# Kernel tuning notes

Hardware: AMD Instinct MI355X
Metric: run time of the kernel (lower is better)

The kernel has to match this reference:

```python
import jax, jax.numpy as jnp
import numpy as np

N_NODES = 50000
N_EDGES = 300000
HID = 256


def setup_inputs() -> dict:
    key = jax.random.key(0)
    ks = jax.random.split(key, 8)
    s = lambda fan_in: 1.0 / np.sqrt(fan_in)
    return {
        "node_embeddings": jax.random.normal(ks[0], (N_NODES, HID), dtype=jnp.float32),
        "edge_index": jax.random.randint(ks[1], (2, N_EDGES), 0, N_NODES, dtype=jnp.int64),
        "edge_attr": jax.random.normal(ks[2], (N_EDGES, 3), dtype=jnp.float32),
        "W1": jax.random.normal(ks[3], (2 * HID + 3, HID), dtype=jnp.float32) * s(2 * HID + 3),
        "b1": jnp.zeros((HID,), dtype=jnp.float32),
        "W2": jax.random.normal(ks[4], (HID, HID // 2), dtype=jnp.float32) * s(HID),
        "b2": jnp.zeros((HID // 2,), dtype=jnp.float32),
        "W3": jax.random.normal(ks[5], (HID // 2, HID // 4), dtype=jnp.float32) * s(HID // 2),
        "b3": jnp.zeros((HID // 4,), dtype=jnp.float32),
        "W4": jax.random.normal(ks[6], (HID // 4, 3), dtype=jnp.float32) * s(HID // 4),
        "b4": jnp.zeros((3,), dtype=jnp.float32),
    }


def reference(node_embeddings, edge_index, edge_attr, W1, b1, W2, b2, W3, b3, W4, b4):
    # Gather source/target node embeddings: [E, H] each
    src = node_embeddings[edge_index[0]]
    dst = node_embeddings[edge_index[1]]
    feats = jnp.concatenate([src, dst, edge_attr], axis=-1)  # [E, 2H+3]
    # edge_encoder: Linear -> ReLU -> (Dropout=identity in eval) -> Linear
    h = jax.nn.relu(feats @ W1 + b1)
    h = h @ W2 + b2  # [E, H//2]
    # classifier: Linear -> ReLU -> Linear
    h = jax.nn.relu(h @ W3 + b3)
    logits = h @ W4 + b4  # [E, 3]
    return logits
```

## Files before the change

kernel.cpp:

```cpp
#include <hip/hip_runtime.h>
#include <hip/hip_bf16.h>
#include <stdint.h>
#include <stddef.h>


#define NN 50000
#define NE 300000
#define KG(kq,g2) ((kq)*2+(g2))

using bf16x8 = __attribute__((ext_vector_type(8))) short;
using f32x16 = __attribute__((ext_vector_type(16))) float;
using f32x4  = __attribute__((ext_vector_type(4))) float;
using f32x2  = __attribute__((ext_vector_type(2))) float;
using u32x4  = __attribute__((ext_vector_type(4))) unsigned int;
using u32x2  = __attribute__((ext_vector_type(2))) unsigned int;

#define OFF_PQ   0ULL
#define SZ_PQ    (50000ULL*512ULL*2ULL)
#define OFF_W1   (OFF_PQ + SZ_PQ)
#define SZ_W1    (512ULL*256ULL*2ULL)
#define OFF_W1C  (OFF_W1 + SZ_W1)
#define SZ_W1C   (3ULL*256ULL*4ULL)
#define OFF_W2   (OFF_W1C + SZ_W1C)
#define SZ_W2    (128ULL*256ULL*2ULL)
#define OFF_W3   (OFF_W2 + SZ_W2)
#define SZ_W3    (64ULL*128ULL*2ULL)
#define OFF_W4   (OFF_W3 + SZ_W3)
#define SZ_W4    (16ULL*64ULL*2ULL)
#define OFF_FLAG (OFF_W4 + SZ_W4)
#define WS_NEED  (OFF_FLAG + 16ULL)

__device__ __forceinline__ unsigned short f2bf(float x){
  unsigned u = __float_as_uint(x);
  unsigned r = 0x7FFFu + ((u >> 16) & 1u);
  return (unsigned short)((u + r) >> 16);
}
__device__ __forceinline__ unsigned cvtpk(float lo, float hi){
  unsigned r;
  asm("v_cvt_pk_bf16_f32 %0, %1, %2" : "=v"(r) : "v"(lo), "v"(hi));
  return r;
}
__device__ __forceinline__ f32x2 unpk(unsigned w){
  f32x2 r;
  r[0] = __uint_as_float(w << 16);
  r[1] = __uint_as_float(w & 0xFFFF0000u);
  return r;
}
__device__ __forceinline__ f32x16 mfma32(bf16x8 a, bf16x8 b, f32x16 c){
  return __builtin_amdgcn_mfma_f32_32x32x16_bf16(a, b, c, 0, 0, 0);
}
__device__ __forceinline__ f32x4 mfma16(bf16x8 a, bf16x8 b, f32x4 c){
  return __builtin_amdgcn_mfma_f32_16x16x32_bf16(a, b, c, 0, 0, 0);
}
__device__ __forceinline__ f32x16 zero16(){
  f32x16 v;
#pragma unroll
  for (int i = 0; i < 16; ++i) v[i] = 0.f;
  return v;
}

__global__ void prep_pack(const float* __restrict__ W1, const float* __restrict__ W2,
                          const float* __restrict__ W3, const float* __restrict__ W4,
                          const int* __restrict__ ei32, char* __restrict__ ws)
{
  int i = blockIdx.x * 256 + threadIdx.x;
  unsigned short* w1i = (unsigned short*)(ws + OFF_W1);
  unsigned short* w2i = (unsigned short*)(ws + OFF_W2);
  unsigned short* w3i = (unsigned short*)(ws + OFF_W3);
  unsigned short* w4i = (unsigned short*)(ws + OFF_W4);

  if (i < 131072){
    int j = i & 7, out = (i >> 3) & 511, kg = i >> 12;
    int k = (kg >> 1)*16 + (kg & 1)*8 + j;
    float v = (out < 256) ? W1[(size_t)k*256 + out]
                          : W1[(size_t)(256 + k)*256 + (out - 256)];
    w1i[i] = f2bf(v);
  } else if (i < 131072 + 32768){
    int i2 = i - 131072;
    int j = i2 & 7, out = (i2 >> 3) & 127, sg = i2 >> 10;
    int k = (sg >> 2)*32 + (sg & 3)*8 + j;
    w2i[i2] = f2bf(W2[(size_t)k*128 + out]);
  } else if (i < 131072 + 32768 + 8192){
    int i3 = i - 131072 - 32768;
    int j = i3 & 7, out = (i3 >> 3) & 63, sg = i3 >> 9;
    int k = (sg >> 2)*32 + (sg & 3)*8 + j;
    w3i[i3] = f2bf(W3[(size_t)k*64 + out]);
  } else if (i < 131072 + 32768 + 8192 + 1024){
    int i4 = i - 131072 - 32768 - 8192;
    int j = i4 & 7, out = (i4 >> 3) & 15, sg = i4 >> 7;
    int k = (sg >> 2)*32 + (sg & 3)*8 + j;
    w4i[i4] = (out < 3) ? f2bf(W4[(size_t)k*3 + out]) : (unsigned short)0;
  }
  if (i < 768){
    float* w1c = (float*)(ws + OFF_W1C);
    w1c[i] = W1[(size_t)(512 + i/256)*256 + (i & 255)];
  }
  if (i == 0){
    int f = 1;
    for (int t = 1; t < 64; t += 2) if (ei32[t] != 0) { f = 0; break; }
    *(int*)(ws + OFF_FLAG) = f;
  }
}

__global__ __launch_bounds__(512, 2) void gemm1(const float* __restrict__ emb,
                                                const float* __restrict__ b1,
                                                char* __restrict__ ws)
{
  __shared__ __align__(16) unsigned short U[16896];

  const int tid = threadIdx.x;
  const int wv = tid >> 6, l = tid & 63, ln = l & 31, g2 = l >> 5;
  const int nb = blockIdx.x * 64;
  const int ob = wv * 64;
  const unsigned short* w1L = (const unsigned short*)(ws + OFF_W1);
  unsigned short* PQ = (unsigned short*)(ws + OFF_PQ);

  bf16x8 aw[2][16];
#pragma unroll
  for (int kq = 0; kq < 16; ++kq){
#pragma unroll
    for (int t2 = 0; t2 < 2; ++t2)
      aw[t2][kq] = *(const bf16x8*)(w1L + ((size_t)KG(kq,g2)*512 + ob + t2*32 + ln)*8);
  }

#pragma unroll
  for (int it = 0; it < 8; ++it){
    int u = it*512 + tid;
    int kg = u >> 7, node = (u >> 1) & 63, half = u & 1;
    int n = nb + node; if (n >= NN) n = NN - 1;
    int k = (kg >> 1)*16 + (kg & 1)*8 + half*4;
    f32x4 e = *(const f32x4*)(emb + (size_t)n*256 + k);
    u32x2 w; w[0] = cvtpk(e[0], e[1]); w[1] = cvtpk(e[2], e[3]);
    *(u32x2*)(U + (size_t)kg*512 + node*8 + half*4) = w;
  }
  __syncthreads();

  f32x16 acc[2][2];
  acc[0][0] = zero16(); acc[0][1] = zero16();
  acc[1][0] = zero16(); acc[1][1] = zero16();
#pragma unroll
  for (int kq = 0; kq < 16; ++kq){
    bf16x8 b0  = *(const bf16x8*)(U + ((size_t)KG(kq,g2)*64 +      ln)*8);
    bf16x8 b1v = *(const bf16x8*)(U + ((size_t)KG(kq,g2)*64 + 32 + ln)*8);
    acc[0][0] = mfma32(aw[0][kq], b0,  acc[0][0]);
    acc[1][0] = mfma32(aw[1][kq], b0,  acc[1][0]);
    acc[0][1] = mfma32(aw[0][kq], b1v, acc[0][1]);
    acc[1][1] = mfma32(aw[1][kq], b1v, acc[1][1]);
  }
  __syncthreads();

  const int r_ = tid >> 4;
  const int j_ = tid & 15;
#define G1PASS(BG)                                                             \
  {                                                                            \
           \
    _Pragma("unroll")                                                          \
    for (int t2 = 0; t2 < 2; ++t2){                                            \
      _Pragma("unroll")                                                        \
      for (int rr = 0; rr < 4; ++rr){                                          \
        int o = ob + t2*32 + rr*8 + g2*4;                                      \
        f32x4 bv = {0.f,0.f,0.f,0.f};                                          \
        if (ob + t2*32 < 256) bv = *(const f32x4*)(b1 + o);                    \
        unsigned d0 = cvtpk(acc[t2][BG][rr*4+0]+bv[0], acc[t2][BG][rr*4+1]+bv[1]); \
        unsigned d1 = cvtpk(acc[t2][BG][rr*4+2]+bv[2], acc[t2][BG][rr*4+3]+bv[3]); \
        u32x2 st = {d0, d1};                                                   \
        *(u32x2*)(U + (size_t)ln*516 + o) = st;                                \
      }                                                                        \
    }                                                                          \
    __syncthreads();                                                           \
                            \
    {                                                                          \
      int n = nb + (BG)*32 + r_;                                               \
      if (n < NN){                                                             \
        _Pragma("unroll")                                                      \
        for (int ii = 0; ii < 4; ++ii){                                        \
          uint4 v = *(const uint4*)(U + (size_t)r_*516 + ii*128 + j_*8);       \
          *(uint4*)(PQ + (size_t)n*512 + ii*128 + j_*8) = v;                   \
        }                                                                      \
      }                                                                        \
    }                                                                          \
  }
  G1PASS(0);
  __syncthreads();
  G1PASS(1);
#undef G1PASS
}


#define PAIRX(LO, HI, D) ((D)==0 ? (f32x2){(LO)[0],(LO)[1]} : \
                          (D)==1 ? (f32x2){(LO)[2],(LO)[3]} : \
                          (D)==2 ? (f32x2){(HI)[0],(HI)[1]} : \
                                   (f32x2){(HI)[2],(HI)[3]})

#define H1BUILD(PC, QC, A0, A1, A2, BOUT)                                      \
  {                                                                            \
    u32x4 pu = __builtin_bit_cast(u32x4, PC);                                  \
    u32x4 qu = __builtin_bit_cast(u32x4, QC);                                  \
    f32x2 z2 = {0.f, 0.f};                                                     \
    unsigned bu0, bu1, bu2, bu3;                                               \
    _Pragma("unroll")                                                          \
    for (int d = 0; d < 4; ++d){                                               \
      f32x2 h = unpk(pu[d]) + unpk(qu[d]);                                     \
      h += PAIRX(w0lo, w0hi, d) * (A0);                                        \
      h += PAIRX(w1lo, w1hi, d) * (A1);                                        \
      h += PAIRX(w2lo, w2hi, d) * (A2);                                        \
      h = __builtin_elementwise_max(h, z2);                                    \
      unsigned c = cvtpk(h[0], h[1]);                                          \
      if (d==0) bu0 = c; else if (d==1) bu1 = c; else if (d==2) bu2 = c;       \
      else bu3 = c;                                                            \
    }                                                                          \
    u32x4 buv = {bu0, bu1, bu2, bu3};                                          \
    BOUT = __builtin_bit_cast(bf16x8, buv);                                    \
  }

#define L2S(S, P0, Q0, P1, Q1)                                                 \
  {                                                                            \
    const int kb = (S)*32 + g4*8;                                              \
    f32x4 w0lo = *(const f32x4*)(w1c_lds +   0 + kb);                          \
    f32x4 w0hi = *(const f32x4*)(w1c_lds +   4 + kb);                          \
    f32x4 w1lo = *(const f32x4*)(w1c_lds + 256 + kb);                          \
    f32x4 w1hi = *(const f32x4*)(w1c_lds + 260 + kb);                          \
    f32x4 w2lo = *(const f32x4*)(w1c_lds + 512 + kb);                          \
    f32x4 w2hi = *(const f32x4*)(w1c_lds + 516 + kb);                          \
    bf16x8 b0, b1;                                                             \
    H1BUILD(P0, Q0, at0e0, at1e0, at2e0, b0);                                  \
    H1BUILD(P1, Q1, at0e1, at1e1, at2e1, b1);                                  \
    if ((S) + 2 <= 7){                                                         \
      P0 = *(const bf16x8*)(Prow0 + ((S)+2)*32);                               \
      Q0 = *(const bf16x8*)(Qrow0 + ((S)+2)*32);                               \
      P1 = *(const bf16x8*)(Prow1 + ((S)+2)*32);                               \
      Q1 = *(const bf16x8*)(Qrow1 + ((S)+2)*32);                               \
    }                                                                          \
    const char* abase = smem + (size_t)((S)*4 + g4)*2048 + c16*16;             \
    _Pragma("unroll")                                                          \
    for (int t = 0; t < 8; ++t){                                               \
      bf16x8 af = *(const bf16x8*)(abase + t*256);                             \
      acc2[t][0] = mfma16(af, b0, acc2[t][0]);                                 \
      acc2[t][1] = mfma16(af, b1, acc2[t][1]);                                 \
    }                                                                          \
  }

__global__ __launch_bounds__(512, 4) void fused(const int* __restrict__ eidx,
                                                const float* __restrict__ attr,
                                                const float* __restrict__ b2,
                                                const float* __restrict__ b3,
                                                const float* __restrict__ b4,
                                                const char* __restrict__ ws,
                                                float* __restrict__ out)
{
  __shared__ __align__(16) char smem[65536 + 3072];
  const int tid = threadIdx.x;
  const int wv = tid >> 6, l = tid & 63, c16 = l & 15, g4 = l >> 4;

  const unsigned short* PQ  = (const unsigned short*)(ws + OFF_PQ);
  const unsigned short* w3g = (const unsigned short*)(ws + OFF_W3);
  const unsigned short* w4g = (const unsigned short*)(ws + OFF_W4);
  const float* W1c = (const float*)(ws + OFF_W1C);
  const int flag64 = *(const int*)(ws + OFF_FLAG);
  const float* w1c_lds = (const float*)(smem + 65536);

  const int ebase = blockIdx.x * 256 + wv * 32;
  const int e0 = ebase + c16,      e1 = ebase + 16 + c16;
  const bool ev0 = (e0 < NE),      ev1 = (e1 < NE);
  const int ec0 = ev0 ? e0 : 0,    ec1 = ev1 ? e1 : 0;
  const int si0 = flag64 ? eidx[2*(size_t)ec0]        : eidx[ec0];
  const int di0 = flag64 ? eidx[2*((size_t)NE + ec0)] : eidx[NE + ec0];
  const int si1 = flag64 ? eidx[2*(size_t)ec1]        : eidx[ec1];
  const int di1 = flag64 ? eidx[2*((size_t)NE + ec1)] : eidx[NE + ec1];

  const float at0e0 = ev0 ? attr[(size_t)ec0*3 + 0] : 0.f;
  const float at1e0 = ev0 ? attr[(size_t)ec0*3 + 1] : 0.f;
  const float at2e0 = ev0 ? attr[(size_t)ec0*3 + 2] : 0.f;
  const float at0e1 = ev1 ? attr[(size_t)ec1*3 + 0] : 0.f;
  const float at1e1 = ev1 ? attr[(size_t)ec1*3 + 1] : 0.f;
  const float at2e1 = ev1 ? attr[(size_t)ec1*3 + 2] : 0.f;

  const unsigned short* Prow0 = PQ + (size_t)si0*512 + g4*8;
  const unsigned short* Qrow0 = PQ + (size_t)di0*512 + 256 + g4*8;
  const unsigned short* Prow1 = PQ + (size_t)si1*512 + g4*8;
  const unsigned short* Qrow1 = PQ + (size_t)di1*512 + 256 + g4*8;

  bf16x8 pA0 = *(const bf16x8*)(Prow0 +  0), qA0 = *(const bf16x8*)(Qrow0 +  0);
  bf16x8 pA1 = *(const bf16x8*)(Prow1 +  0), qA1 = *(const bf16x8*)(Qrow1 +  0);
  bf16x8 pB0 = *(const bf16x8*)(Prow0 + 32), qB0 = *(const bf16x8*)(Qrow0 + 32);
  bf16x8 pB1 = *(const bf16x8*)(Prow1 + 32), qB1 = *(const bf16x8*)(Qrow1 + 32);

  {
    const uint4* src = (const uint4*)(ws + OFF_W2);
    uint4* dst = (uint4*)smem;
#pragma unroll
    for (int it = 0; it < 8; ++it) dst[it*512 + tid] = src[it*512 + tid];
    if (tid < 192) ((f32x4*)(smem + 65536))[tid] = ((const f32x4*)W1c)[tid];
  }
  __syncthreads();

  f32x4 acc2[8][2];
#pragma unroll
  for (int t = 0; t < 8; ++t){ acc2[t][0] = (f32x4){0,0,0,0}; acc2[t][1] = (f32x4){0,0,0,0}; }

  L2S(0, pA0, qA0, pA1, qA1);
  L2S(1, pB0, qB0, pB1, qB1);
  L2S(2, pA0, qA0, pA1, qA1);
  L2S(3, pB0, qB0, pB1, qB1);
  L2S(4, pA0, qA0, pA1, qA1);
  L2S(5, pB0, qB0, pB1, qB1);
  L2S(6, pA0, qA0, pA1, qA1);
  L2S(7, pB0, qB0, pB1, qB1);

  __syncthreads();

  unsigned short* hslot = (unsigned short*)(smem + wv*8192);
#pragma unroll
  for (int t = 0; t < 8; ++t){
    f32x4 bv = *(const f32x4*)(b2 + t*16 + g4*4);
    const int sg_o = t*2 + (g4 >> 1);
    const int j0 = (g4 & 1)*4;
#pragma unroll
    for (int g = 0; g < 2; ++g){
      unsigned d0 = cvtpk(acc2[t][g][0]+bv[0], acc2[t][g][1]+bv[1]);
      unsigned d1 = cvtpk(acc2[t][g][2]+bv[2], acc2[t][g][3]+bv[3]);
      u32x2 st = {d0, d1};
      *(u32x2*)(hslot + ((sg_o*32 + g*16 + c16)*8 + j0)) = st;
    }
  }

  f32x4 acc3[4][2];
#pragma unroll
  for (int t = 0; t < 4; ++t){ acc3[t][0] = (f32x4){0,0,0,0}; acc3[t][1] = (f32x4){0,0,0,0}; }
#pragma unroll
  for (int ks = 0; ks < 4; ++ks){
    const int sg = ks*4 + g4;
    bf16x8 bb0 = *(const bf16x8*)(hslot + (sg*32 +      c16)*8);
    bf16x8 bb1 = *(const bf16x8*)(hslot + (sg*32 + 16 + c16)*8);
#pragma unroll
    for (int t = 0; t < 4; ++t){
      bf16x8 af = *(const bf16x8*)(w3g + ((size_t)sg*64 + t*16 + c16)*8);
      acc3[t][0] = mfma16(af, bb0, acc3[t][0]);
      acc3[t][1] = mfma16(af, bb1, acc3[t][1]);
    }
  }

#pragma unroll
  for (int t = 0; t < 4; ++t){
    f32x4 bv = *(const f32x4*)(b3 + t*16 + g4*4);
    const int sg_o = t*2 + (g4 >> 1);
    const int j0 = (g4 & 1)*4;
#pragma unroll
    for (int g = 0; g < 2; ++g){
      unsigned d0 = cvtpk(fmaxf(acc3[t][g][0]+bv[0],0.f), fmaxf(acc3[t][g][1]+bv[1],0.f));
      unsigned d1 = cvtpk(fmaxf(acc3[t][g][2]+bv[2],0.f), fmaxf(acc3[t][g][3]+bv[3],0.f));
      u32x2 st = {d0, d1};
      *(u32x2*)(hslot + ((sg_o*32 + g*16 + c16)*8 + j0)) = st;
    }
  }

  f32x4 acc40 = {0,0,0,0}, acc41 = {0,0,0,0};
#pragma unroll
  for (int ks = 0; ks < 2; ++ks){
    const int sg = ks*4 + g4;
    bf16x8 af = *(const bf16x8*)(w4g + ((size_t)sg*16 + c16)*8);
    bf16x8 bb0 = *(const bf16x8*)(hslot + (sg*32 +      c16)*8);
    bf16x8 bb1 = *(const bf16x8*)(hslot + (sg*32 + 16 + c16)*8);
    acc40 = mfma16(af, bb0, acc40);
    acc41 = mfma16(af, bb1, acc41);
  }
  if (g4 == 0){
    float c0 = b4[0], c1 = b4[1], c2 = b4[2];
    if (ev0){
      out[(size_t)e0*3 + 0] = acc40[0] + c0;
      out[(size_t)e0*3 + 1] = acc40[1] + c1;
      out[(size_t)e0*3 + 2] = acc40[2] + c2;
    }
    if (ev1){
      out[(size_t)e1*3 + 0] = acc41[0] + c0;
      out[(size_t)e1*3 + 1] = acc41[1] + c1;
      out[(size_t)e1*3 + 2] = acc41[2] + c2;
    }
  }
}

extern "C" void kernel_launch(void* const* d_in, const int* in_sizes, int n_in,
                              void* d_out, int out_size, void* d_ws, size_t ws_size,
                              hipStream_t stream)
{
  const float* emb  = (const float*)d_in[0];
  const int*   eidx = (const int*)  d_in[1];
  const float* attr = (const float*)d_in[2];
  const float* W1   = (const float*)d_in[3];
  const float* b1   = (const float*)d_in[4];
  const float* W2   = (const float*)d_in[5];
  const float* b2   = (const float*)d_in[6];
  const float* W3   = (const float*)d_in[7];
  const float* b3   = (const float*)d_in[8];
  const float* W4   = (const float*)d_in[9];
  const float* b4   = (const float*)d_in[10];
  char* ws = (char*)d_ws;
  float* out = (float*)d_out;

  if (ws_size < WS_NEED) return;

  prep_pack<<<676, 256, 0, stream>>>(W1, W2, W3, W4, eidx, ws);
  gemm1<<<(NN + 63)/64, 512, 0, stream>>>(emb, b1, ws);
  fused<<<(NE + 255)/256, 512, 0, stream>>>(eidx, attr, b2, b3, b4, ws, out);
}
```

Measured before the change: 116.7 us.

## Move small weight packing into gemm1, process two node tiles per block, add setprio

Packing of the W2, W3, W4 and W1-tail weights moves out of prep_pack into extra blocks of gemm1, so prep_pack only converts W1. Each gemm1 block now handles two 64-node tiles in a loop, so the W1 fragments held in registers are loaded once and reused across both tiles. The grid shrinks to about one wave of blocks. The fused kernel wraps its MFMA loops in s_setprio to favour matrix issue. The risks are less parallelism in gemm1 and extra synchronisation, and the setprio effect depends on how waves interleave.

```diff
diff --git a/kernel.cpp b/kernel.cpp
--- a/kernel.cpp
+++ b/kernel.cpp
@@ -7,6 +7,7 @@
 #define NN 50000
 #define NE 300000
 #define KG(kq,g2) ((kq)*2+(g2))
+#define NBG1 391
 
 using bf16x8 = __attribute__((ext_vector_type(8))) short;
 using f32x16 = __attribute__((ext_vector_type(16))) float;
@@ -59,41 +60,17 @@
   return v;
 }
 
-__global__ void prep_pack(const float* __restrict__ W1, const float* __restrict__ W2,
-                          const float* __restrict__ W3, const float* __restrict__ W4,
+__global__ void prep_pack(const float* __restrict__ W1,
                           const int* __restrict__ ei32, char* __restrict__ ws)
 {
   int i = blockIdx.x * 256 + threadIdx.x;
   unsigned short* w1i = (unsigned short*)(ws + OFF_W1);
-  unsigned short* w2i = (unsigned short*)(ws + OFF_W2);
-  unsigned short* w3i = (unsigned short*)(ws + OFF_W3);
-  unsigned short* w4i = (unsigned short*)(ws + OFF_W4);
-
   if (i < 131072){
     int j = i & 7, out = (i >> 3) & 511, kg = i >> 12;
     int k = (kg >> 1)*16 + (kg & 1)*8 + j;
     float v = (out < 256) ? W1[(size_t)k*256 + out]
                           : W1[(size_t)(256 + k)*256 + (out - 256)];
     w1i[i] = f2bf(v);
-  } else if (i < 131072 + 32768){
-    int i2 = i - 131072;
-    int j = i2 & 7, out = (i2 >> 3) & 127, sg = i2 >> 10;
-    int k = (sg >> 2)*32 + (sg & 3)*8 + j;
-    w2i[i2] = f2bf(W2[(size_t)k*128 + out]);
-  } else if (i < 131072 + 32768 + 8192){
-    int i3 = i - 131072 - 32768;
-    int j = i3 & 7, out = (i3 >> 3) & 63, sg = i3 >> 9;
-    int k = (sg >> 2)*32 + (sg & 3)*8 + j;
-    w3i[i3] = f2bf(W3[(size_t)k*64 + out]);
-  } else if (i < 131072 + 32768 + 8192 + 1024){
-    int i4 = i - 131072 - 32768 - 8192;
-    int j = i4 & 7, out = (i4 >> 3) & 15, sg = i4 >> 7;
-    int k = (sg >> 2)*32 + (sg & 3)*8 + j;
-    w4i[i4] = (out < 3) ? f2bf(W4[(size_t)k*3 + out]) : (unsigned short)0;
-  }
-  if (i < 768){
-    float* w1c = (float*)(ws + OFF_W1C);
-    w1c[i] = W1[(size_t)(512 + i/256)*256 + (i & 255)];
   }
   if (i == 0){
     int f = 1;
@@ -104,13 +81,45 @@
 
 __global__ __launch_bounds__(512, 2) void gemm1(const float* __restrict__ emb,
                                                 const float* __restrict__ b1,
+                                                const float* __restrict__ W1,
+                                                const float* __restrict__ W2,
+                                                const float* __restrict__ W3,
+                                                const float* __restrict__ W4,
                                                 char* __restrict__ ws)
 {
   __shared__ __align__(16) unsigned short U[16896];
 
   const int tid = threadIdx.x;
+  const int bid = blockIdx.x;
+
+  if (bid >= NBG1){
+    int p = (bid - NBG1)*512 + tid;
+    unsigned short* w2i = (unsigned short*)(ws + OFF_W2);
+    unsigned short* w3i = (unsigned short*)(ws + OFF_W3);
+    unsigned short* w4i = (unsigned short*)(ws + OFF_W4);
+    float* w1c = (float*)(ws + OFF_W1C);
+    if (p < 32768){
+      int j = p & 7, out = (p >> 3) & 127, sg = p >> 10;
+      int k = (sg >> 2)*32 + (sg & 3)*8 + j;
+      w2i[p] = f2bf(W2[(size_t)k*128 + out]);
+    } else if (p < 40960){
+      int i3 = p - 32768;
+      int j = i3 & 7, out = (i3 >> 3) & 63, sg = i3 >> 9;
+      int k = (sg >> 2)*32 + (sg & 3)*8 + j;
+      w3i[i3] = f2bf(W3[(size_t)k*64 + out]);
+    } else if (p < 41984){
+      int i4 = p - 40960;
+      int j = i4 & 7, out = (i4 >> 3) & 15, sg = i4 >> 7;
+      int k = (sg >> 2)*32 + (sg & 3)*8 + j;
+      w4i[i4] = (out < 3) ? f2bf(W4[(size_t)k*3 + out]) : (unsigned short)0;
+    } else if (p < 42752){
+      int i5 = p - 41984;
+      w1c[i5] = W1[(size_t)(512 + i5/256)*256 + (i5 & 255)];
+    }
+    return;
+  }
+
   const int wv = tid >> 6, l = tid & 63, ln = l & 31, g2 = l >> 5;
-  const int nb = blockIdx.x * 64;
   const int ob = wv * 64;
   const unsigned short* w1L = (const unsigned short*)(ws + OFF_W1);
   unsigned short* PQ = (unsigned short*)(ws + OFF_PQ);
@@ -123,67 +132,71 @@
       aw[t2][kq] = *(const bf16x8*)(w1L + ((size_t)KG(kq,g2)*512 + ob + t2*32 + ln)*8);
   }
 
-#pragma unroll
-  for (int it = 0; it < 8; ++it){
-    int u = it*512 + tid;
-    int kg = u >> 7, node = (u >> 1) & 63, half = u & 1;
-    int n = nb + node; if (n >= NN) n = NN - 1;
-    int k = (kg >> 1)*16 + (kg & 1)*8 + half*4;
-    f32x4 e = *(const f32x4*)(emb + (size_t)n*256 + k);
-    u32x2 w; w[0] = cvtpk(e[0], e[1]); w[1] = cvtpk(e[2], e[3]);
-    *(u32x2*)(U + (size_t)kg*512 + node*8 + half*4) = w;
-  }
-  __syncthreads();
-
-  f32x16 acc[2][2];
-  acc[0][0] = zero16(); acc[0][1] = zero16();
-  acc[1][0] = zero16(); acc[1][1] = zero16();
-#pragma unroll
-  for (int kq = 0; kq < 16; ++kq){
-    bf16x8 b0  = *(const bf16x8*)(U + ((size_t)KG(kq,g2)*64 +      ln)*8);
-    bf16x8 b1v = *(const bf16x8*)(U + ((size_t)KG(kq,g2)*64 + 32 + ln)*8);
-    acc[0][0] = mfma32(aw[0][kq], b0,  acc[0][0]);
-    acc[1][0] = mfma32(aw[1][kq], b0,  acc[1][0]);
-    acc[0][1] = mfma32(aw[0][kq], b1v, acc[0][1]);
-    acc[1][1] = mfma32(aw[1][kq], b1v, acc[1][1]);
-  }
-  __syncthreads();
-
-  const int r_ = tid >> 4;
-  const int j_ = tid & 15;
+#pragma unroll 1
+  for (int rep = 0; rep < 2; ++rep){
+    const int nb = (bid*2 + rep) * 64;
+    __syncthreads();
+
+#pragma unroll
+    for (int it = 0; it < 8; ++it){
+      int u = it*512 + tid;
+      int kg = u >> 7, node = (u >> 1) & 63, half = u & 1;
+      int n = nb + node; if (n >= NN) n = NN - 1;
+      int k = (kg >> 1)*16 + (kg & 1)*8 + half*4;
+      f32x4 e = *(const f32x4*)(emb + (size_t)n*256 + k);
+      u32x2 w; w[0] = cvtpk(e[0], e[1]); w[1] = cvtpk(e[2], e[3]);
+      *(u32x2*)(U + (size_t)kg*512 + node*8 + half*4) = w;
+    }
+    __syncthreads();
+
+    f32x16 acc[2][2];
+    acc[0][0] = zero16(); acc[0][1] = zero16();
+    acc[1][0] = zero16(); acc[1][1] = zero16();
+#pragma unroll
+    for (int kq = 0; kq < 16; ++kq){
+      bf16x8 b0  = *(const bf16x8*)(U + ((size_t)KG(kq,g2)*64 +      ln)*8);
+      bf16x8 b1v = *(const bf16x8*)(U + ((size_t)KG(kq,g2)*64 + 32 + ln)*8);
+      acc[0][0] = mfma32(aw[0][kq], b0,  acc[0][0]);
+      acc[1][0] = mfma32(aw[1][kq], b0,  acc[1][0]);
+      acc[0][1] = mfma32(aw[0][kq], b1v, acc[0][1]);
+      acc[1][1] = mfma32(aw[1][kq], b1v, acc[1][1]);
+    }
+    __syncthreads();
+
+    const int r_ = tid >> 4;
+    const int j_ = tid & 15;
 #define G1PASS(BG)                                                             \
-  {                                                                            \
-           \
-    _Pragma("unroll")                                                          \
-    for (int t2 = 0; t2 < 2; ++t2){                                            \
+    {                                                                          \
       _Pragma("unroll")                                                        \
-      for (int rr = 0; rr < 4; ++rr){                                          \
-        int o = ob + t2*32 + rr*8 + g2*4;                                      \
-        f32x4 bv = {0.f,0.f,0.f,0.f};                                          \
-        if (ob + t2*32 < 256) bv = *(const f32x4*)(b1 + o);                    \
-        unsigned d0 = cvtpk(acc[t2][BG][rr*4+0]+bv[0], acc[t2][BG][rr*4+1]+bv[1]); \
-        unsigned d1 = cvtpk(acc[t2][BG][rr*4+2]+bv[2], acc[t2][BG][rr*4+3]+bv[3]); \
-        u32x2 st = {d0, d1};                                                   \
-        *(u32x2*)(U + (size_t)ln*516 + o) = st;                                \
-      }                                                                        \
-    }                                                                          \
-    __syncthreads();                                                           \
-                            \
-    {                                                                          \
-      int n = nb + (BG)*32 + r_;                                               \
-      if (n < NN){                                                             \
+      for (int t2 = 0; t2 < 2; ++t2){                                          \
         _Pragma("unroll")                                                      \
-        for (int ii = 0; ii < 4; ++ii){                                        \
-          uint4 v = *(const uint4*)(U + (size_t)r_*516 + ii*128 + j_*8);       \
-          *(uint4*)(PQ + (size_t)n*512 + ii*128 + j_*8) = v;                   \
+        for (int rr = 0; rr < 4; ++rr){                                        \
+          int o = ob + t2*32 + rr*8 + g2*4;                                    \
+          f32x4 bv = {0.f,0.f,0.f,0.f};                                        \
+          if (ob + t2*32 < 256) bv = *(const f32x4*)(b1 + o);                  \
+          unsigned d0 = cvtpk(acc[t2][BG][rr*4+0]+bv[0], acc[t2][BG][rr*4+1]+bv[1]); \
+          unsigned d1 = cvtpk(acc[t2][BG][rr*4+2]+bv[2], acc[t2][BG][rr*4+3]+bv[3]); \
+          u32x2 st = {d0, d1};                                                 \
+          *(u32x2*)(U + (size_t)ln*516 + o) = st;                              \
         }                                                                      \
       }                                                                        \
-    }                                                                          \
-  }
-  G1PASS(0);
-  __syncthreads();
-  G1PASS(1);
+      __syncthreads();                                                         \
+      {                                                                        \
+        int n = nb + (BG)*32 + r_;                                             \
+        if (n < NN){                                                           \
+          _Pragma("unroll")                                                    \
+          for (int ii = 0; ii < 4; ++ii){                                      \
+            uint4 v = *(const uint4*)(U + (size_t)r_*516 + ii*128 + j_*8);     \
+            *(uint4*)(PQ + (size_t)n*512 + ii*128 + j_*8) = v;                 \
+          }                                                                    \
+        }                                                                      \
+      }                                                                        \
+    }
+    G1PASS(0);
+    __syncthreads();
+    G1PASS(1);
 #undef G1PASS
+  }
 }
 
 
@@ -232,12 +245,14 @@
       Q1 = *(const bf16x8*)(Qrow1 + ((S)+2)*32);                               \
     }                                                                          \
     const char* abase = smem + (size_t)((S)*4 + g4)*2048 + c16*16;             \
+    __builtin_amdgcn_s_setprio(1);                                             \
     _Pragma("unroll")                                                          \
     for (int t = 0; t < 8; ++t){                                               \
       bf16x8 af = *(const bf16x8*)(abase + t*256);                             \
       acc2[t][0] = mfma16(af, b0, acc2[t][0]);                                 \
       acc2[t][1] = mfma16(af, b1, acc2[t][1]);                                 \
     }                                                                          \
+    __builtin_amdgcn_s_setprio(0);                                             \
   }
 
 __global__ __launch_bounds__(512, 4) void fused(const int* __restrict__ eidx,
@@ -332,12 +347,14 @@
     const int sg = ks*4 + g4;
     bf16x8 bb0 = *(const bf16x8*)(hslot + (sg*32 +      c16)*8);
     bf16x8 bb1 = *(const bf16x8*)(hslot + (sg*32 + 16 + c16)*8);
+    __builtin_amdgcn_s_setprio(1);
 #pragma unroll
     for (int t = 0; t < 4; ++t){
       bf16x8 af = *(const bf16x8*)(w3g + ((size_t)sg*64 + t*16 + c16)*8);
       acc3[t][0] = mfma16(af, bb0, acc3[t][0]);
       acc3[t][1] = mfma16(af, bb1, acc3[t][1]);
     }
+    __builtin_amdgcn_s_setprio(0);
   }
 
 #pragma unroll
@@ -399,7 +416,7 @@
 
   if (ws_size < WS_NEED) return;
 
-  prep_pack<<<676, 256, 0, stream>>>(W1, W2, W3, W4, eidx, ws);
-  gemm1<<<(NN + 63)/64, 512, 0, stream>>>(emb, b1, ws);
+  prep_pack<<<512, 256, 0, stream>>>(W1, eidx, ws);
+  gemm1<<<NBG1 + 84, 512, 0, stream>>>(emb, b1, W1, W2, W3, W4, ws);
   fused<<<(NE + 255)/256, 512, 0, stream>>>(eidx, attr, b2, b3, b4, ws, out);
 }
```

Measured after the change: 240.8 us. 106% more time.
